# Kernel optimization log

Hardware: AMD Instinct MI355X
Metric: run time of the kernel (lower is better)

## Reference

```python
import jax, jax.numpy as jnp
import numpy as np

B, L, D = 8, 128, 768
DEP, POS = 64, 64
OUT = 768
NEG = -1e30


def setup_inputs() -> dict:
    key = jax.random.key(0)
    ks = jax.random.split(key, 12)
    fan = DEP + POS + D
    s_attn = 1.0 / np.sqrt(fan)
    inp = {
        "text": jax.random.normal(ks[0], (B, L, D), jnp.float32),
        "adj": jax.random.randint(ks[1], (B, L, L), 0, 2, jnp.int32),
        "dep_embed": jax.random.normal(ks[2], (B, L, L, DEP), jnp.float32),
        "pos_embed": jax.random.normal(ks[3], (B, L, POS), jnp.float32),
        # dep_attn Linear(dep+pos+in -> out), split into the three column blocks
        # of the concat order [text | pos | dep]
        "Wt": jax.random.normal(ks[4], (D, OUT), jnp.float32) * s_attn,
        "Wp_attn": jax.random.normal(ks[5], (POS, OUT), jnp.float32) * s_attn,
        "Wd_attn": jax.random.normal(ks[6], (DEP, OUT), jnp.float32) * s_attn,
        "b_attn": jax.random.normal(ks[7], (OUT,), jnp.float32) * s_attn,
        # dep_fc Linear(dep -> out)
        "Wd": jax.random.normal(ks[8], (DEP, OUT), jnp.float32) / np.sqrt(DEP),
        "bd": jax.random.normal(ks[9], (OUT,), jnp.float32) / np.sqrt(DEP),
        # pos_fc Linear(pos -> out)
        "Wp": jax.random.normal(ks[10], (POS, OUT), jnp.float32) / np.sqrt(POS),
        "bp": jax.random.normal(ks[11], (OUT,), jnp.float32) / np.sqrt(POS),
    }
    return inp


def reference(text, adj, dep_embed, pos_embed, Wt, Wp_attn, Wd_attn, b_attn, Wd, bd, Wp, bp):
    # dep_attn(cat([val_us, pos_us, dep_embed])) == sum of per-block linears,
    # with the text/pos parts broadcast along the j (neighbor) axis.
    r = (jnp.einsum('bid,do->bio', text, Wt)[:, :, None, :]
         + jnp.einsum('bip,po->bio', pos_embed, Wp_attn)[:, :, None, :]
         + jnp.einsum('bijd,do->bijo', dep_embed, Wd_attn)
         + b_attn)                                    # [B, L, L, OUT]
    scores = jnp.sum(r, axis=-1) + jnp.where(adj == 0, NEG, 0.0)
    p = jax.nn.softmax(scores, axis=2)                # [B, L, L]
    # output = val_us + pos_fc(pos_us) + dep_fc(dep_embed); weighted-sum over j
    msg = (text[:, :, None, :]
           + (pos_embed @ Wp + bp)[:, :, None, :]
           + jnp.einsum('bijd,do->bijo', dep_embed, Wd) + bd)  # [B, L, L, D]
    output_sum = jnp.einsum('bij,bijo->bio', p, msg)  # [B, L, D]
    return r, output_sum, p
```

## Files before the change

kernel.cpp:

```cpp
#include <hip/hip_runtime.h>
#include <hip/hip_bf16.h>

typedef float v4f __attribute__((ext_vector_type(4)));
typedef short short8 __attribute__((ext_vector_type(8)));

__device__ inline ushort f2bf(float x) {
    unsigned u = __float_as_uint(x);
    unsigned r = u + 0x7fffu + ((u >> 16) & 1u);
    return (ushort)(r >> 16);
}

__global__ __launch_bounds__(256) void k_wdsum(const float* __restrict__ Wda,
                                               float* __restrict__ wd_sum) {
    int k = blockIdx.x, t = threadIdx.x;
    float s = Wda[k * 768 + t] + Wda[k * 768 + 256 + t] + Wda[k * 768 + 512 + t];
#pragma unroll
    for (int off = 32; off; off >>= 1) s += __shfl_down(s, off, 64);
    __shared__ float red[4];
    if ((t & 63) == 0) red[t >> 6] = s;
    __syncthreads();
    if (t == 0) wd_sum[k] = red[0] + red[1] + red[2] + red[3];
}

__global__ __launch_bounds__(256) void k_cvt(const float* __restrict__ Wda,
                                             ushort* __restrict__ wdat) {
    int idx = blockIdx.x * 256 + threadIdx.x;
    int o = idx >> 6, k = idx & 63;
    wdat[idx] = f2bf(Wda[(size_t)k * 768 + o]);
}

__global__ __launch_bounds__(256) void k_tattn(const float* __restrict__ text,
                                               const float* __restrict__ pos,
                                               const float* __restrict__ Wt,
                                               const float* __restrict__ Wpa,
                                               const float* __restrict__ b_attn,
                                               float* __restrict__ t_attn) {
    __shared__ float At[64][68];
    __shared__ float Bt[64][64];
    int t = threadIdx.x;
    int M0 = blockIdx.x * 64, N0 = blockIdx.y * 64;
    int r0 = (t >> 4) * 4, o0 = (t & 15) * 4;
    float acc[16] = {};
    for (int kc = 0; kc < 13; ++kc) {
        __syncthreads();
        for (int f = t * 4; f < 4096; f += 1024) {
            int row = f >> 6, kcol = f & 63;
            float4 v;
            if (kc < 12) v = *(const float4*)&text[(size_t)(M0 + row) * 768 + kc * 64 + kcol];
            else         v = *(const float4*)&pos[(size_t)(M0 + row) * 64 + kcol];
            At[kcol + 0][row] = v.x; At[kcol + 1][row] = v.y;
            At[kcol + 2][row] = v.z; At[kcol + 3][row] = v.w;
        }
        for (int f = t * 4; f < 4096; f += 1024) {
            int kr = f >> 6, oc = f & 63;
            float4 v;
            if (kc < 12) v = *(const float4*)&Wt[(size_t)(kc * 64 + kr) * 768 + N0 + oc];
            else         v = *(const float4*)&Wpa[(size_t)kr * 768 + N0 + oc];
            *(float4*)&Bt[kr][oc] = v;
        }
        __syncthreads();
#pragma unroll 8
        for (int k = 0; k < 64; ++k) {
            float4 a = *(const float4*)&At[k][r0];
            float4 b = *(const float4*)&Bt[k][o0];
            float av[4] = {a.x, a.y, a.z, a.w};
            float bv[4] = {b.x, b.y, b.z, b.w};
#pragma unroll
            for (int i = 0; i < 4; ++i)
#pragma unroll
                for (int j = 0; j < 4; ++j) acc[i * 4 + j] += av[i] * bv[j];
        }
    }
    float4 bias = *(const float4*)&b_attn[N0 + o0];
    float bb[4] = {bias.x, bias.y, bias.z, bias.w};
#pragma unroll
    for (int i = 0; i < 4; ++i) {
        float4 o;
        o.x = acc[i * 4 + 0] + bb[0]; o.y = acc[i * 4 + 1] + bb[1];
        o.z = acc[i * 4 + 2] + bb[2]; o.w = acc[i * 4 + 3] + bb[3];
        *(float4*)&t_attn[(size_t)(M0 + r0 + i) * 768 + N0 + o0] = o;
    }
}

__global__ __launch_bounds__(256) void k_mega(const float* __restrict__ dep,
                                              const int* __restrict__ adj,
                                              const ushort* __restrict__ wdat,
                                              const float* __restrict__ t_attn,
                                              const float* __restrict__ wd_sum,
                                              float* __restrict__ r_out,
                                              float* __restrict__ out_p,
                                              float* __restrict__ pd_out) {
    __shared__ __align__(16) ushort db[128 * 72];
    __shared__ float wds[64];
    __shared__ float sc[128];
    __shared__ float pv[128];
    __shared__ float pdp[4][64];
    __shared__ float red[8];
    int t = threadIdx.x;
    int bi = blockIdx.x;
    const float* depb = dep + (size_t)bi * (128 * 64);
#pragma unroll
    for (int it = 0; it < 8; ++it) {
        int f = t + it * 256;
        int j = f >> 4, k4 = f & 15;
        float4 v = *(const float4*)&depb[(size_t)f * 4];
        union { ushort u[4]; uint2 d; } pk;
        pk.u[0] = f2bf(v.x); pk.u[1] = f2bf(v.y);
        pk.u[2] = f2bf(v.z); pk.u[3] = f2bf(v.w);
        *(uint2*)&db[j * 72 + k4 * 4] = pk.d;
    }
    if (t < 64) wds[t] = wd_sum[t];
    const float* ta = t_attn + (size_t)bi * 768;
    float s = ta[t] + ta[t + 256] + ta[t + 512];
#pragma unroll
    for (int off = 32; off; off >>= 1) s += __shfl_down(s, off, 64);
    if ((t & 63) == 0) red[t >> 6] = s;
    __syncthreads();
    float S_t = red[0] + red[1] + red[2] + red[3];
    if (t < 128) {
        const float* row = depb + (size_t)t * 64;
        float d = 0.f;
#pragma unroll
        for (int k4 = 0; k4 < 16; ++k4) {
            float4 v = *(const float4*)&row[k4 * 4];
            d += v.x * wds[k4 * 4 + 0] + v.y * wds[k4 * 4 + 1]
               + v.z * wds[k4 * 4 + 2] + v.w * wds[k4 * 4 + 3];
        }
        float sval = S_t + d;
        if (adj[(size_t)bi * 128 + t] == 0) sval += -1e30f;
        sc[t] = sval;
    }
    __syncthreads();
    if (t < 64) {
        float v = fmaxf(sc[t], sc[t + 64]);
#pragma unroll
        for (int off = 32; off; off >>= 1) v = fmaxf(v, __shfl_down(v, off, 64));
        if (t == 0) red[4] = v;
    }
    __syncthreads();
    if (t < 128) pv[t] = __expf(sc[t] - red[4]);
    __syncthreads();
    if (t < 64) {
        float v = pv[t] + pv[t + 64];
#pragma unroll
        for (int off = 32; off; off >>= 1) v += __shfl_down(v, off, 64);
        if (t == 0) red[5] = v;
    }
    __syncthreads();
    float inv = 1.0f / red[5];
    if (t < 128) {
        float pj = pv[t] * inv;
        pv[t] = pj;
        out_p[(size_t)bi * 128 + t] = pj;
    }
    __syncthreads();
    {
        int kk = t & 63, seg = t >> 6;
        float a = 0.f;
#pragma unroll
        for (int jj = 0; jj < 32; ++jj)
            a += pv[seg * 32 + jj] * depb[(size_t)(seg * 32 + jj) * 64 + kk];
        pdp[seg][kk] = a;
    }
    __syncthreads();
    if (t < 64) pd_out[(size_t)bi * 64 + t] = pdp[0][t] + pdp[1][t] + pdp[2][t] + pdp[3][t];

    int w = t >> 6, l = t & 63;
    int col = l & 15, q = l >> 4;
    short8 afr[2][2];
#pragma unroll
    for (int jt = 0; jt < 2; ++jt)
#pragma unroll
        for (int h = 0; h < 2; ++h)
            afr[jt][h] = *(const short8*)&db[(w * 32 + jt * 16 + col) * 72 + h * 32 + q * 8];
    float* rb = r_out + (size_t)bi * (128 * 768);
    for (int oc = 0; oc < 12; ++oc) {
        int O = oc * 64;
        short8 bfr[4][2];
#pragma unroll
        for (int ot = 0; ot < 4; ++ot)
#pragma unroll
            for (int h = 0; h < 2; ++h)
                bfr[ot][h] = *(const short8*)&wdat[(size_t)(O + ot * 16 + col) * 64 + h * 32 + q * 8];
        float tav[4];
#pragma unroll
        for (int ot = 0; ot < 4; ++ot) tav[ot] = ta[O + ot * 16 + col];
#pragma unroll
        for (int ot = 0; ot < 4; ++ot) {
#pragma unroll
            for (int jt = 0; jt < 2; ++jt) {
                v4f acc = {0.f, 0.f, 0.f, 0.f};
                acc = __builtin_amdgcn_mfma_f32_16x16x32_bf16(afr[jt][0], bfr[ot][0], acc, 0, 0, 0);
                acc = __builtin_amdgcn_mfma_f32_16x16x32_bf16(afr[jt][1], bfr[ot][1], acc, 0, 0, 0);
                float* dst = rb + (size_t)(w * 32 + jt * 16 + q * 4) * 768 + O + ot * 16 + col;
#pragma unroll
                for (int reg = 0; reg < 4; ++reg)
                    __builtin_nontemporal_store(acc[reg] + tav[ot], dst + (size_t)reg * 768);
            }
        }
    }
}

__global__ __launch_bounds__(256) void k_out(const float* __restrict__ text,
                                             const float* __restrict__ pos,
                                             const float* __restrict__ Wp,
                                             const float* __restrict__ bp,
                                             const float* __restrict__ Wd,
                                             const float* __restrict__ bd,
                                             const float* __restrict__ pd,
                                             float* __restrict__ outp) {
    __shared__ float ps[8][64];
    __shared__ float pdl[8][64];
    int t = threadIdx.x;
    int bi0 = blockIdx.x * 8;
    for (int f = t; f < 512; f += 256) {
        int g = f >> 6, k = f & 63;
        ps[g][k]  = pos[(size_t)(bi0 + g) * 64 + k];
        pdl[g][k] = pd[(size_t)(bi0 + g) * 64 + k];
    }
    __syncthreads();
    if (t < 192) {
        int d0 = t * 4;
        float acc[32] = {};
#pragma unroll 4
        for (int k = 0; k < 64; ++k) {
            float4 wp = *(const float4*)&Wp[(size_t)k * 768 + d0];
            float4 wd = *(const float4*)&Wd[(size_t)k * 768 + d0];
            float wpv[4] = {wp.x, wp.y, wp.z, wp.w};
            float wdv[4] = {wd.x, wd.y, wd.z, wd.w};
#pragma unroll
            for (int g = 0; g < 8; ++g) {
                float pk = ps[g][k], dk = pdl[g][k];
#pragma unroll
                for (int c = 0; c < 4; ++c) acc[g * 4 + c] += pk * wpv[c] + dk * wdv[c];
            }
        }
        float4 bpv = *(const float4*)&bp[d0];
        float4 bdv = *(const float4*)&bd[d0];
        float bb[4] = {bpv.x + bdv.x, bpv.y + bdv.y, bpv.z + bdv.z, bpv.w + bdv.w};
#pragma unroll
        for (int g = 0; g < 8; ++g) {
            float4 tx = *(const float4*)&text[(size_t)(bi0 + g) * 768 + d0];
            float4 o;
            o.x = acc[g * 4 + 0] + tx.x + bb[0];
            o.y = acc[g * 4 + 1] + tx.y + bb[1];
            o.z = acc[g * 4 + 2] + tx.z + bb[2];
            o.w = acc[g * 4 + 3] + tx.w + bb[3];
            *(float4*)&outp[(size_t)(bi0 + g) * 768 + d0] = o;
        }
    }
}

extern "C" void kernel_launch(void* const* d_in, const int* in_sizes, int n_in,
                              void* d_out, int out_size, void* d_ws, size_t ws_size,
                              hipStream_t stream) {
    const float* text   = (const float*)d_in[0];
    const int*   adj    = (const int*)d_in[1];
    const float* dep    = (const float*)d_in[2];
    const float* pos    = (const float*)d_in[3];
    const float* Wt     = (const float*)d_in[4];
    const float* Wpa    = (const float*)d_in[5];
    const float* Wda    = (const float*)d_in[6];
    const float* b_attn = (const float*)d_in[7];
    const float* Wd     = (const float*)d_in[8];
    const float* bd     = (const float*)d_in[9];
    const float* Wp     = (const float*)d_in[10];
    const float* bp     = (const float*)d_in[11];

    float* out    = (float*)d_out;
    float* r_out  = out;
    float* os_out = out + (size_t)8 * 128 * 128 * 768;
    float* p_out  = os_out + (size_t)8 * 128 * 768;

    float* ws     = (float*)d_ws;
    float* t_attn = ws;
    float* wd_sum = ws + 786432;
    float* pd     = ws + 786496;
    ushort* wdat  = (ushort*)(ws + 852032);

    k_wdsum<<<64, 256, 0, stream>>>(Wda, wd_sum);
    k_cvt<<<192, 256, 0, stream>>>(Wda, wdat);
    k_tattn<<<dim3(16, 12), 256, 0, stream>>>(text, pos, Wt, Wpa, b_attn, t_attn);
    k_mega<<<1024, 256, 0, stream>>>(dep, adj, wdat, t_attn, wd_sum, r_out, p_out, pd);
    k_out<<<128, 256, 0, stream>>>(text, pos, Wp, bp, Wd, bd, pd, os_out);
}
```

Baseline: 620.1 us.

## Merge prep kernels, vectorize r stores via swapped MFMA operands, split k_out finer

```diff
diff --git a/kernel.cpp b/kernel.cpp
--- a/kernel.cpp
+++ b/kernel.cpp
@@ -10,35 +10,36 @@
     return (ushort)(r >> 16);
 }
 
-__global__ __launch_bounds__(256) void k_wdsum(const float* __restrict__ Wda,
-                                               float* __restrict__ wd_sum) {
-    int k = blockIdx.x, t = threadIdx.x;
-    float s = Wda[k * 768 + t] + Wda[k * 768 + 256 + t] + Wda[k * 768 + 512 + t];
-#pragma unroll
-    for (int off = 32; off; off >>= 1) s += __shfl_down(s, off, 64);
-    __shared__ float red[4];
-    if ((t & 63) == 0) red[t >> 6] = s;
-    __syncthreads();
-    if (t == 0) wd_sum[k] = red[0] + red[1] + red[2] + red[3];
-}
-
-__global__ __launch_bounds__(256) void k_cvt(const float* __restrict__ Wda,
-                                             ushort* __restrict__ wdat) {
-    int idx = blockIdx.x * 256 + threadIdx.x;
-    int o = idx >> 6, k = idx & 63;
-    wdat[idx] = f2bf(Wda[(size_t)k * 768 + o]);
-}
-
-__global__ __launch_bounds__(256) void k_tattn(const float* __restrict__ text,
-                                               const float* __restrict__ pos,
-                                               const float* __restrict__ Wt,
-                                               const float* __restrict__ Wpa,
-                                               const float* __restrict__ b_attn,
-                                               float* __restrict__ t_attn) {
+__global__ __launch_bounds__(256) void k_prep(const float* __restrict__ text,
+                                              const float* __restrict__ pos,
+                                              const float* __restrict__ Wt,
+                                              const float* __restrict__ Wpa,
+                                              const float* __restrict__ b_attn,
+                                              const float* __restrict__ Wda,
+                                              float* __restrict__ t_attn,
+                                              float* __restrict__ wd_sum,
+                                              ushort* __restrict__ wdat) {
     __shared__ float At[64][68];
     __shared__ float Bt[64][64];
     int t = threadIdx.x;
-    int M0 = blockIdx.x * 64, N0 = blockIdx.y * 64;
+    int bid = blockIdx.x;
+    if (bid >= 192) {
+        int k = bid - 192;
+        float a0 = Wda[(size_t)k * 768 + t];
+        float a1 = Wda[(size_t)k * 768 + 256 + t];
+        float a2 = Wda[(size_t)k * 768 + 512 + t];
+        wdat[(size_t)t * 64 + k]         = f2bf(a0);
+        wdat[(size_t)(t + 256) * 64 + k] = f2bf(a1);
+        wdat[(size_t)(t + 512) * 64 + k] = f2bf(a2);
+        float s = a0 + a1 + a2;
+#pragma unroll
+        for (int off = 32; off; off >>= 1) s += __shfl_down(s, off, 64);
+        if ((t & 63) == 0) At[0][t >> 6] = s;
+        __syncthreads();
+        if (t == 0) wd_sum[k] = At[0][0] + At[0][1] + At[0][2] + At[0][3];
+        return;
+    }
+    int M0 = (bid & 15) * 64, N0 = (bid >> 4) * 64;
     int r0 = (t >> 4) * 4, o0 = (t & 15) * 4;
     float acc[16] = {};
     for (int kc = 0; kc < 13; ++kc) {
@@ -182,20 +183,23 @@
 #pragma unroll
             for (int h = 0; h < 2; ++h)
                 bfr[ot][h] = *(const short8*)&wdat[(size_t)(O + ot * 16 + col) * 64 + h * 32 + q * 8];
-        float tav[4];
-#pragma unroll
-        for (int ot = 0; ot < 4; ++ot) tav[ot] = ta[O + ot * 16 + col];
+        float4 tav[4];
+#pragma unroll
+        for (int ot = 0; ot < 4; ++ot) tav[ot] = *(const float4*)&ta[O + ot * 16 + q * 4];
 #pragma unroll
         for (int ot = 0; ot < 4; ++ot) {
 #pragma unroll
             for (int jt = 0; jt < 2; ++jt) {
                 v4f acc = {0.f, 0.f, 0.f, 0.f};
-                acc = __builtin_amdgcn_mfma_f32_16x16x32_bf16(afr[jt][0], bfr[ot][0], acc, 0, 0, 0);
-                acc = __builtin_amdgcn_mfma_f32_16x16x32_bf16(afr[jt][1], bfr[ot][1], acc, 0, 0, 0);
-                float* dst = rb + (size_t)(w * 32 + jt * 16 + q * 4) * 768 + O + ot * 16 + col;
-#pragma unroll
-                for (int reg = 0; reg < 4; ++reg)
-                    __builtin_nontemporal_store(acc[reg] + tav[ot], dst + (size_t)reg * 768);
+                acc = __builtin_amdgcn_mfma_f32_16x16x32_bf16(bfr[ot][0], afr[jt][0], acc, 0, 0, 0);
+                acc = __builtin_amdgcn_mfma_f32_16x16x32_bf16(bfr[ot][1], afr[jt][1], acc, 0, 0, 0);
+                v4f o4;
+                o4[0] = acc[0] + tav[ot].x;
+                o4[1] = acc[1] + tav[ot].y;
+                o4[2] = acc[2] + tav[ot].z;
+                o4[3] = acc[3] + tav[ot].w;
+                v4f* dst = (v4f*)(rb + (size_t)(w * 32 + jt * 16 + col) * 768 + O + ot * 16 + q * 4);
+                __builtin_nontemporal_store(o4, dst);
             }
         }
     }
@@ -209,19 +213,19 @@
                                              const float* __restrict__ bd,
                                              const float* __restrict__ pd,
                                              float* __restrict__ outp) {
-    __shared__ float ps[8][64];
-    __shared__ float pdl[8][64];
+    __shared__ float ps[4][64];
+    __shared__ float pdl[4][64];
     int t = threadIdx.x;
-    int bi0 = blockIdx.x * 8;
-    for (int f = t; f < 512; f += 256) {
-        int g = f >> 6, k = f & 63;
+    int bi0 = blockIdx.x * 4;
+    {
+        int g = t >> 6, k = t & 63;
         ps[g][k]  = pos[(size_t)(bi0 + g) * 64 + k];
         pdl[g][k] = pd[(size_t)(bi0 + g) * 64 + k];
     }
     __syncthreads();
     if (t < 192) {
         int d0 = t * 4;
-        float acc[32] = {};
+        float acc[16] = {};
 #pragma unroll 4
         for (int k = 0; k < 64; ++k) {
             float4 wp = *(const float4*)&Wp[(size_t)k * 768 + d0];
@@ -229,7 +233,7 @@
             float wpv[4] = {wp.x, wp.y, wp.z, wp.w};
             float wdv[4] = {wd.x, wd.y, wd.z, wd.w};
 #pragma unroll
-            for (int g = 0; g < 8; ++g) {
+            for (int g = 0; g < 4; ++g) {
                 float pk = ps[g][k], dk = pdl[g][k];
 #pragma unroll
                 for (int c = 0; c < 4; ++c) acc[g * 4 + c] += pk * wpv[c] + dk * wdv[c];
@@ -239,7 +243,7 @@
         float4 bdv = *(const float4*)&bd[d0];
         float bb[4] = {bpv.x + bdv.x, bpv.y + bdv.y, bpv.z + bdv.z, bpv.w + bdv.w};
 #pragma unroll
-        for (int g = 0; g < 8; ++g) {
+        for (int g = 0; g < 4; ++g) {
             float4 tx = *(const float4*)&text[(size_t)(bi0 + g) * 768 + d0];
             float4 o;
             o.x = acc[g * 4 + 0] + tx.x + bb[0];
@@ -278,9 +282,7 @@
     float* pd     = ws + 786496;
     ushort* wdat  = (ushort*)(ws + 852032);
 
-    k_wdsum<<<64, 256, 0, stream>>>(Wda, wd_sum);
-    k_cvt<<<192, 256, 0, stream>>>(Wda, wdat);
-    k_tattn<<<dim3(16, 12), 256, 0, stream>>>(text, pos, Wt, Wpa, b_attn, t_attn);
+    k_prep<<<256, 256, 0, stream>>>(text, pos, Wt, Wpa, b_attn, Wda, t_attn, wd_sum, wdat);
     k_mega<<<1024, 256, 0, stream>>>(dep, adj, wdat, t_attn, wd_sum, r_out, p_out, pd);
-    k_out<<<128, 256, 0, stream>>>(text, pos, Wp, bp, Wd, bd, pd, os_out);
-}
+    k_out<<<256, 256, 0, stream>>>(text, pos, Wp, bp, Wd, bd, pd, os_out);
+}
```

Measured after the change: 621.1 us. No clear change (+0.1%).
